# Optimization experiments

Measured on AMD Instinct MI355X. Metric: run time of the kernel, lower is better.

## Reference

```python
import jax, jax.numpy as jnp
import numpy as np

NG, G = 256, 32          # num groups, pedestrians per group
E, H, MID, BN_EPS = 64, 64, 512, 1e-5
BOT = 32

def _bn(x, gamma, beta):
    # training-mode BatchNorm1d applied PER GROUP (axis=1 are the rows of
    # that group's pairwise batch), biased variance, eps=1e-5
    mean = jnp.mean(x, axis=1, keepdims=True)
    var = jnp.mean((x - mean) ** 2, axis=1, keepdims=True)
    return gamma * (x - mean) * jax.lax.rsqrt(var + BN_EPS) + beta

def setup_inputs() -> dict:
    key = jax.random.key(0)
    ks = jax.random.split(key, 8)
    B = NG * G
    starts = np.arange(NG, dtype=np.int64) * G
    seq_start_end = jnp.asarray(np.stack([starts, starts + G], axis=1))
    def lin(k, fi, fo):
        kw, kb = jax.random.split(k)
        lim = 1.0 / np.sqrt(fi)
        return (jax.random.uniform(kw, (fi, fo), jnp.float32, -lim, lim),
                jax.random.uniform(kb, (fo,), jnp.float32, -lim, lim))
    W_spatial, b_spatial = lin(ks[0], 2, E)
    W1, b1 = lin(ks[1], E + H, MID)
    W2, b2 = lin(ks[2], MID, BOT)
    return {
        'h_states': jax.random.normal(ks[3], (1, B, H), jnp.float32),
        'seq_start_end': seq_start_end,
        'end_pos': jax.random.normal(ks[4], (B, 2), jnp.float32),
        'W_spatial': W_spatial, 'b_spatial': b_spatial,
        'W1': W1, 'b1': b1,
        'gamma1': jnp.ones((MID,), jnp.float32), 'beta1': jnp.zeros((MID,), jnp.float32),
        'W2': W2, 'b2': b2,
        'gamma2': jnp.ones((BOT,), jnp.float32), 'beta2': jnp.zeros((BOT,), jnp.float32),
    }

def reference(h_states, seq_start_end, end_pos, W_spatial, b_spatial,
              W1, b1, gamma1, beta1, W2, b2, gamma2, beta2):
    B = end_pos.shape[0]
    ng = seq_start_end.shape[0]
    g = B // ng  # equal-size groups -> fully vectorized
    h = h_states.reshape(B, H).reshape(ng, g, H)
    pos = end_pos.reshape(ng, g, 2)
    # rel[n, i, j] = pos[n, j] - pos[n, i]  (matches repeat/tile in torch code)
    rel = pos[:, None, :, :] - pos[:, :, None, :]            # (ng, g, g, 2)
    emb = rel @ W_spatial + b_spatial                         # (ng, g, g, E)
    hb = jnp.broadcast_to(h[:, None, :, :], (ng, g, g, H))    # hidden of ped j
    x = jnp.concatenate([emb, hb], axis=-1).reshape(ng, g * g, E + H)
    x = jax.nn.relu(_bn(x @ W1 + b1, gamma1, beta1))          # (ng, g*g, 512)
    x = jax.nn.relu(_bn(x @ W2 + b2, gamma2, beta2))          # (ng, g*g, 32)
    pool = x.reshape(ng, g, g, BOT).max(axis=2)               # max over j
    return pool.reshape(B, BOT)
```

## Files before the change

### kernel.cpp

```cpp
#include <hip/hip_runtime.h>

#define GRP 32
#define HD 64
#define MIDD 512
#define LDSTR 520

typedef _Float16 half8 __attribute__((ext_vector_type(8)));
typedef float floatx4 __attribute__((ext_vector_type(4)));

__device__ inline half8 relu8(half8 x) {
    return __builtin_elementwise_max(x, (half8)(_Float16)0);
}

__global__ void prep_wr(const float* __restrict__ Ws, const float* __restrict__ W1,
                        float* __restrict__ wr) {
    int c = blockIdx.x * 64 + threadIdx.x;
    float a0 = 0.f, a1 = 0.f;
#pragma unroll
    for (int e = 0; e < 64; ++e) {
        float w = W1[e * MIDD + c];
        a0 = fmaf(Ws[e], w, a0);
        a1 = fmaf(Ws[64 + e], w, a1);
    }
    wr[c] = a0;
    wr[MIDD + c] = a1;
}

__launch_bounds__(512, 2)
__global__ void pool_main(const float* __restrict__ h_states,
                          const float* __restrict__ end_pos,
                          const float* __restrict__ W1,
                          const float* __restrict__ gamma1,
                          const float* __restrict__ beta1,
                          const float* __restrict__ W2,
                          const float* __restrict__ gamma2,
                          const float* __restrict__ beta2,
                          const float* __restrict__ wr,
                          float* __restrict__ out) {
    __shared__ _Float16 Ash[32][LDSTR];
    __shared__ _Float16 Bsh[32][LDSTR];
    __shared__ _Float16 w2T[32][LDSTR];
    __shared__ float posx[32], posy[32];
    __shared__ float wr0s[512], wr1s[512], g1s[512], be1s[512];
    __shared__ float red[8][2][16][2];
    __shared__ float bns[32], bno[32];

    const int tid  = threadIdx.x;
    const int wave = tid >> 6;
    const int lane = tid & 63;
    const int quad = lane >> 4;
    const int n16  = lane & 15;
    const int g0   = blockIdx.x * GRP;

    wr0s[tid] = wr[tid];
    wr1s[tid] = wr[512 + tid];
    g1s[tid]  = gamma1[tid];
    be1s[tid] = beta1[tid];
    if (tid < 32) {
        posx[tid] = end_pos[(g0 + tid) * 2];
        posy[tid] = end_pos[(g0 + tid) * 2 + 1];
    }
#pragma unroll
    for (int it = 0; it < 32; ++it) {
        int idx = tid + it * 512;
        int k = idx >> 5, nn = idx & 31;
        w2T[nn][k] = (_Float16)W2[idx];
    }
    __syncthreads();

    {
        half8 afr[2][2];
#pragma unroll
        for (int mt = 0; mt < 2; ++mt)
#pragma unroll
            for (int kk = 0; kk < 2; ++kk) {
                const float4* hp = (const float4*)(h_states + (size_t)(g0 + mt * 16 + n16) * HD + kk * 32 + quad * 8);
                float4 p0 = hp[0], p1 = hp[1];
                half8 a;
                a[0] = (_Float16)p0.x; a[1] = (_Float16)p0.y; a[2] = (_Float16)p0.z; a[3] = (_Float16)p0.w;
                a[4] = (_Float16)p1.x; a[5] = (_Float16)p1.y; a[6] = (_Float16)p1.z; a[7] = (_Float16)p1.w;
                afr[mt][kk] = a;
            }

        floatx4 acc[2][4];
#pragma unroll
        for (int a = 0; a < 2; ++a)
#pragma unroll
            for (int b = 0; b < 4; ++b) acc[a][b] = (floatx4){0.f, 0.f, 0.f, 0.f};

#pragma unroll
        for (int nt4 = 0; nt4 < 4; ++nt4) {
            const int c = (wave * 4 + nt4) * 16 + n16;
#pragma unroll
            for (int kk = 0; kk < 2; ++kk) {
                half8 b;
#pragma unroll
                for (int x = 0; x < 8; ++x) {
                    int k = kk * 32 + quad * 8 + x;
                    b[x] = (_Float16)W1[(size_t)(64 + k) * MIDD + c];
                }
#pragma unroll
                for (int mt = 0; mt < 2; ++mt)
                    acc[mt][nt4] = __builtin_amdgcn_mfma_f32_16x16x32_f16(afr[mt][kk], b, acc[mt][nt4], 0, 0, 0);
            }
        }

#pragma unroll
        for (int nt4 = 0; nt4 < 4; ++nt4) {
            const int c = (wave * 4 + nt4) * 16 + n16;
            const float w0 = wr0s[c], w1 = wr1s[c];

            float su = 0.f, ssu = 0.f;
#pragma unroll
            for (int mt = 0; mt < 2; ++mt)
#pragma unroll
                for (int r = 0; r < 4; ++r) {
                    int j = mt * 16 + quad * 4 + r;
                    float u = acc[mt][nt4][r] + posx[j] * w0 + posy[j] * w1;
                    acc[mt][nt4][r] = u;
                    su += u;
                    ssu = fmaf(u, u, ssu);
                }
            su  += __shfl_xor(su, 16);  su  += __shfl_xor(su, 32);
            ssu += __shfl_xor(ssu, 16); ssu += __shfl_xor(ssu, 32);

            float vv[8];
            float sv = 0.f, ssv = 0.f;
#pragma unroll
            for (int ii = 0; ii < 8; ++ii) {
                int i = quad * 8 + ii;
                float v = posx[i] * w0 + posy[i] * w1;
                vv[ii] = v;
                sv += v;
                ssv = fmaf(v, v, ssv);
            }
            sv  += __shfl_xor(sv, 16);  sv  += __shfl_xor(sv, 32);
            ssv += __shfl_xor(ssv, 16); ssv += __shfl_xor(ssv, 32);

            const float muu = su * (1.f / 32.f), muv = sv * (1.f / 32.f);
            const float var = (ssu * (1.f / 32.f) - muu * muu) + (ssv * (1.f / 32.f) - muv * muv);
            const float s    = g1s[c] * rsqrtf(var + 1e-5f);
            const float boff = s * (muu - muv) - be1s[c];

#pragma unroll
            for (int mt = 0; mt < 2; ++mt)
#pragma unroll
                for (int r = 0; r < 4; ++r) {
                    int j = mt * 16 + quad * 4 + r;
                    Ash[j][c] = (_Float16)(s * acc[mt][nt4][r]);
                }
#pragma unroll
            for (int ii = 0; ii < 8; ++ii)
                Bsh[quad * 8 + ii][c] = (_Float16)fmaf(s, vv[ii], boff);
        }
    }
    __syncthreads();

    floatx4 acc2[8][2];
#pragma unroll
    for (int a = 0; a < 8; ++a)
#pragma unroll
        for (int b = 0; b < 2; ++b) acc2[a][b] = (floatx4){0.f, 0.f, 0.f, 0.f};

#pragma unroll 2
    for (int kk = 0; kk < 16; ++kk) {
        const int kb = kk * 32 + quad * 8;
        const half8 w2f0 = *(const half8*)&w2T[n16][kb];
        const half8 w2f1 = *(const half8*)&w2T[16 + n16][kb];
        const half8 a0 = *(const half8*)&Ash[n16][kb];
        const half8 a1 = *(const half8*)&Ash[16 + n16][kb];
#pragma unroll
        for (int mp = 0; mp < 4; ++mp) {
            const int i = wave * 4 + mp;
            const half8 bf = *(const half8*)&Bsh[i][kb];
            const half8 z0 = relu8(a0 - bf);
            const half8 z1 = relu8(a1 - bf);
            acc2[2 * mp][0]     = __builtin_amdgcn_mfma_f32_16x16x32_f16(z0, w2f0, acc2[2 * mp][0], 0, 0, 0);
            acc2[2 * mp][1]     = __builtin_amdgcn_mfma_f32_16x16x32_f16(z0, w2f1, acc2[2 * mp][1], 0, 0, 0);
            acc2[2 * mp + 1][0] = __builtin_amdgcn_mfma_f32_16x16x32_f16(z1, w2f0, acc2[2 * mp + 1][0], 0, 0, 0);
            acc2[2 * mp + 1][1] = __builtin_amdgcn_mfma_f32_16x16x32_f16(z1, w2f1, acc2[2 * mp + 1][1], 0, 0, 0);
        }
    }

    float s0 = 0.f, q0 = 0.f, s1 = 0.f, q1 = 0.f;
#pragma unroll
    for (int mt = 0; mt < 8; ++mt)
#pragma unroll
        for (int r = 0; r < 4; ++r) {
            float v0 = acc2[mt][0][r], v1 = acc2[mt][1][r];
            s0 += v0; q0 = fmaf(v0, v0, q0);
            s1 += v1; q1 = fmaf(v1, v1, q1);
        }
    s0 += __shfl_xor(s0, 16); s0 += __shfl_xor(s0, 32);
    q0 += __shfl_xor(q0, 16); q0 += __shfl_xor(q0, 32);
    s1 += __shfl_xor(s1, 16); s1 += __shfl_xor(s1, 32);
    q1 += __shfl_xor(q1, 16); q1 += __shfl_xor(q1, 32);
    if (lane < 16) {
        red[wave][0][lane][0] = s0; red[wave][0][lane][1] = q0;
        red[wave][1][lane][0] = s1; red[wave][1][lane][1] = q1;
    }
    __syncthreads();
    if (tid < 32) {
        const int nt = tid >> 4, n = tid & 15;
        float s = 0.f, q = 0.f;
#pragma unroll
        for (int w = 0; w < 8; ++w) { s += red[w][nt][n][0]; q += red[w][nt][n][1]; }
        const float mu  = s * (1.f / 1024.f);
        const float var = q * (1.f / 1024.f) - mu * mu;
        const float sc  = gamma2[tid] * rsqrtf(var + 1e-5f);
        bns[tid] = sc;
        bno[tid] = beta2[tid] - sc * mu;
    }
    __syncthreads();

#pragma unroll
    for (int nt = 0; nt < 2; ++nt) {
        const int c = nt * 16 + n16;
        const float sc = bns[c], off = bno[c];
#pragma unroll
        for (int a = 0; a < 4; ++a) {
            float m = 0.f;
#pragma unroll
            for (int p = 0; p < 2; ++p)
#pragma unroll
                for (int r = 0; r < 4; ++r)
                    m = fmaxf(m, fmaf(sc, acc2[2 * a + p][nt][r], off));
            m = fmaxf(m, __shfl_xor(m, 16));
            m = fmaxf(m, __shfl_xor(m, 32));
            if (quad == nt) {
                const int i = wave * 4 + a;
                out[(size_t)(g0 + i) * 32 + c] = m;
            }
        }
    }
}

extern "C" void kernel_launch(void* const* d_in, const int* in_sizes, int n_in,
                              void* d_out, int out_size, void* d_ws, size_t ws_size,
                              hipStream_t stream) {
    (void)in_sizes; (void)n_in; (void)out_size; (void)ws_size;
    const float* h_states  = (const float*)d_in[0];
    const float* end_pos   = (const float*)d_in[2];
    const float* W_spatial = (const float*)d_in[3];
    const float* W1        = (const float*)d_in[5];
    const float* gamma1    = (const float*)d_in[7];
    const float* beta1     = (const float*)d_in[8];
    const float* W2        = (const float*)d_in[9];
    const float* gamma2    = (const float*)d_in[11];
    const float* beta2     = (const float*)d_in[12];
    float* out = (float*)d_out;
    float* wr  = (float*)d_ws;

    prep_wr<<<dim3(8), dim3(64), 0, stream>>>(W_spatial, W1, wr);
    pool_main<<<dim3(256), dim3(512), 0, stream>>>(h_states, end_pos, W1, gamma1, beta1,
                                                   W2, gamma2, beta2, wr, out);
}
```

Before: 99.23 us.

## Split hidden-state GEMM into a separate pre-kernel writing fp16 intermediate

Moves the h·W1 projection out of the main pooling kernel into a new first kernel that writes an fp16 (B×512) intermediate Q to workspace. The wr precompute is folded into that kernel as an extra block. The main kernel now reads Q and computes the BN1 statistics with one thread per column and a serial loop over 32 rows. The goal is to shorten the main kernel and drop the strided per-block W1 loads, at the cost of an extra 8 MB round trip through global memory. It also creates a race: block 256 writes wr inside the same launch, but other blocks do not read wr, so ordering is still correct.

```diff
diff --git a/kernel.cpp b/kernel.cpp
--- a/kernel.cpp
+++ b/kernel.cpp
@@ -12,36 +12,94 @@
     return __builtin_elementwise_max(x, (half8)(_Float16)0);
 }
 
-__global__ void prep_wr(const float* __restrict__ Ws, const float* __restrict__ W1,
-                        float* __restrict__ wr) {
-    int c = blockIdx.x * 64 + threadIdx.x;
-    float a0 = 0.f, a1 = 0.f;
-#pragma unroll
-    for (int e = 0; e < 64; ++e) {
-        float w = W1[e * MIDD + c];
-        a0 = fmaf(Ws[e], w, a0);
-        a1 = fmaf(Ws[64 + e], w, a1);
-    }
-    wr[c] = a0;
-    wr[MIDD + c] = a1;
+__global__ __launch_bounds__(512) void k1(const float* __restrict__ h_states,
+                                          const float* __restrict__ Ws,
+                                          const float* __restrict__ W1,
+                                          _Float16* __restrict__ Q,
+                                          float* __restrict__ wr) {
+    const int tid  = threadIdx.x;
+    if (blockIdx.x == 256) {
+        const int c = tid;
+        float a0 = 0.f, a1 = 0.f;
+#pragma unroll
+        for (int e = 0; e < 64; ++e) {
+            float w = W1[e * MIDD + c];
+            a0 = fmaf(Ws[e], w, a0);
+            a1 = fmaf(Ws[64 + e], w, a1);
+        }
+        wr[c] = a0;
+        wr[MIDD + c] = a1;
+        return;
+    }
+    const int wave = tid >> 6;
+    const int lane = tid & 63;
+    const int quad = lane >> 4;
+    const int n16  = lane & 15;
+    const int r0 = (blockIdx.x >> 3) * 256 + wave * 32;
+    const int c0 = (blockIdx.x & 7) * 64;
+
+    half8 afr[2][2];
+#pragma unroll
+    for (int mt = 0; mt < 2; ++mt)
+#pragma unroll
+        for (int kk = 0; kk < 2; ++kk) {
+            const float4* hp = (const float4*)(h_states + (size_t)(r0 + mt * 16 + n16) * HD + kk * 32 + quad * 8);
+            float4 p0 = hp[0], p1 = hp[1];
+            half8 a;
+            a[0] = (_Float16)p0.x; a[1] = (_Float16)p0.y; a[2] = (_Float16)p0.z; a[3] = (_Float16)p0.w;
+            a[4] = (_Float16)p1.x; a[5] = (_Float16)p1.y; a[6] = (_Float16)p1.z; a[7] = (_Float16)p1.w;
+            afr[mt][kk] = a;
+        }
+
+    floatx4 acc[2][4];
+#pragma unroll
+    for (int a = 0; a < 2; ++a)
+#pragma unroll
+        for (int b = 0; b < 4; ++b) acc[a][b] = (floatx4){0.f, 0.f, 0.f, 0.f};
+
+#pragma unroll
+    for (int nt = 0; nt < 4; ++nt) {
+        const int c = c0 + nt * 16 + n16;
+#pragma unroll
+        for (int kk = 0; kk < 2; ++kk) {
+            half8 b;
+#pragma unroll
+            for (int x = 0; x < 8; ++x) {
+                int k = kk * 32 + quad * 8 + x;
+                b[x] = (_Float16)W1[(size_t)(64 + k) * MIDD + c];
+            }
+#pragma unroll
+            for (int mt = 0; mt < 2; ++mt)
+                acc[mt][nt] = __builtin_amdgcn_mfma_f32_16x16x32_f16(afr[mt][kk], b, acc[mt][nt], 0, 0, 0);
+        }
+    }
+
+#pragma unroll
+    for (int mt = 0; mt < 2; ++mt)
+#pragma unroll
+        for (int nt = 0; nt < 4; ++nt)
+#pragma unroll
+            for (int r = 0; r < 4; ++r) {
+                int row = r0 + mt * 16 + quad * 4 + r;
+                int c   = c0 + nt * 16 + n16;
+                Q[(size_t)row * MIDD + c] = (_Float16)acc[mt][nt][r];
+            }
 }
 
 __launch_bounds__(512, 2)
-__global__ void pool_main(const float* __restrict__ h_states,
-                          const float* __restrict__ end_pos,
-                          const float* __restrict__ W1,
+__global__ void pool_main(const float* __restrict__ end_pos,
+                          const _Float16* __restrict__ Q,
+                          const float* __restrict__ wr,
                           const float* __restrict__ gamma1,
                           const float* __restrict__ beta1,
                           const float* __restrict__ W2,
                           const float* __restrict__ gamma2,
                           const float* __restrict__ beta2,
-                          const float* __restrict__ wr,
                           float* __restrict__ out) {
     __shared__ _Float16 Ash[32][LDSTR];
     __shared__ _Float16 Bsh[32][LDSTR];
     __shared__ _Float16 w2T[32][LDSTR];
     __shared__ float posx[32], posy[32];
-    __shared__ float wr0s[512], wr1s[512], g1s[512], be1s[512];
     __shared__ float red[8][2][16][2];
     __shared__ float bns[32], bno[32];
 
@@ -52,10 +110,6 @@
     const int n16  = lane & 15;
     const int g0   = blockIdx.x * GRP;
 
-    wr0s[tid] = wr[tid];
-    wr1s[tid] = wr[512 + tid];
-    g1s[tid]  = gamma1[tid];
-    be1s[tid] = beta1[tid];
     if (tid < 32) {
         posx[tid] = end_pos[(g0 + tid) * 2];
         posy[tid] = end_pos[(g0 + tid) * 2 + 1];
@@ -69,89 +123,39 @@
     __syncthreads();
 
     {
-        half8 afr[2][2];
-#pragma unroll
-        for (int mt = 0; mt < 2; ++mt)
-#pragma unroll
-            for (int kk = 0; kk < 2; ++kk) {
-                const float4* hp = (const float4*)(h_states + (size_t)(g0 + mt * 16 + n16) * HD + kk * 32 + quad * 8);
-                float4 p0 = hp[0], p1 = hp[1];
-                half8 a;
-                a[0] = (_Float16)p0.x; a[1] = (_Float16)p0.y; a[2] = (_Float16)p0.z; a[3] = (_Float16)p0.w;
-                a[4] = (_Float16)p1.x; a[5] = (_Float16)p1.y; a[6] = (_Float16)p1.z; a[7] = (_Float16)p1.w;
-                afr[mt][kk] = a;
-            }
-
-        floatx4 acc[2][4];
-#pragma unroll
-        for (int a = 0; a < 2; ++a)
-#pragma unroll
-            for (int b = 0; b < 4; ++b) acc[a][b] = (floatx4){0.f, 0.f, 0.f, 0.f};
-
-#pragma unroll
-        for (int nt4 = 0; nt4 < 4; ++nt4) {
-            const int c = (wave * 4 + nt4) * 16 + n16;
-#pragma unroll
-            for (int kk = 0; kk < 2; ++kk) {
-                half8 b;
-#pragma unroll
-                for (int x = 0; x < 8; ++x) {
-                    int k = kk * 32 + quad * 8 + x;
-                    b[x] = (_Float16)W1[(size_t)(64 + k) * MIDD + c];
-                }
-#pragma unroll
-                for (int mt = 0; mt < 2; ++mt)
-                    acc[mt][nt4] = __builtin_amdgcn_mfma_f32_16x16x32_f16(afr[mt][kk], b, acc[mt][nt4], 0, 0, 0);
-            }
-        }
-
-#pragma unroll
-        for (int nt4 = 0; nt4 < 4; ++nt4) {
-            const int c = (wave * 4 + nt4) * 16 + n16;
-            const float w0 = wr0s[c], w1 = wr1s[c];
-
-            float su = 0.f, ssu = 0.f;
-#pragma unroll
-            for (int mt = 0; mt < 2; ++mt)
-#pragma unroll
-                for (int r = 0; r < 4; ++r) {
-                    int j = mt * 16 + quad * 4 + r;
-                    float u = acc[mt][nt4][r] + posx[j] * w0 + posy[j] * w1;
-                    acc[mt][nt4][r] = u;
-                    su += u;
-                    ssu = fmaf(u, u, ssu);
-                }
-            su  += __shfl_xor(su, 16);  su  += __shfl_xor(su, 32);
-            ssu += __shfl_xor(ssu, 16); ssu += __shfl_xor(ssu, 32);
-
-            float vv[8];
-            float sv = 0.f, ssv = 0.f;
-#pragma unroll
-            for (int ii = 0; ii < 8; ++ii) {
-                int i = quad * 8 + ii;
-                float v = posx[i] * w0 + posy[i] * w1;
-                vv[ii] = v;
-                sv += v;
-                ssv = fmaf(v, v, ssv);
-            }
-            sv  += __shfl_xor(sv, 16);  sv  += __shfl_xor(sv, 32);
-            ssv += __shfl_xor(ssv, 16); ssv += __shfl_xor(ssv, 32);
-
-            const float muu = su * (1.f / 32.f), muv = sv * (1.f / 32.f);
-            const float var = (ssu * (1.f / 32.f) - muu * muu) + (ssv * (1.f / 32.f) - muv * muv);
-            const float s    = g1s[c] * rsqrtf(var + 1e-5f);
-            const float boff = s * (muu - muv) - be1s[c];
-
-#pragma unroll
-            for (int mt = 0; mt < 2; ++mt)
-#pragma unroll
-                for (int r = 0; r < 4; ++r) {
-                    int j = mt * 16 + quad * 4 + r;
-                    Ash[j][c] = (_Float16)(s * acc[mt][nt4][r]);
-                }
-#pragma unroll
-            for (int ii = 0; ii < 8; ++ii)
-                Bsh[quad * 8 + ii][c] = (_Float16)fmaf(s, vv[ii], boff);
+        const int c = tid;
+        const float w0 = wr[c], w1 = wr[MIDD + c];
+        const float g  = gamma1[c], be = beta1[c];
+        const _Float16* qp = Q + (size_t)g0 * MIDD + c;
+
+        float uu[32];
+        float su = 0.f, ssu = 0.f;
+#pragma unroll
+        for (int j = 0; j < 32; ++j) {
+            float u = (float)qp[(size_t)j * MIDD] + posx[j] * w0 + posy[j] * w1;
+            uu[j] = u;
+            su += u;
+            ssu = fmaf(u, u, ssu);
+        }
+        float sv = 0.f, ssv = 0.f;
+#pragma unroll
+        for (int i = 0; i < 32; ++i) {
+            float v = posx[i] * w0 + posy[i] * w1;
+            sv += v;
+            ssv = fmaf(v, v, ssv);
+        }
+        const float muu = su * (1.f / 32.f), muv = sv * (1.f / 32.f);
+        const float var = (ssu * (1.f / 32.f) - muu * muu) + (ssv * (1.f / 32.f) - muv * muv);
+        const float s    = g * rsqrtf(var + 1e-5f);
+        const float boff = s * (muu - muv) - be;
+
+#pragma unroll
+        for (int j = 0; j < 32; ++j)
+            Ash[j][c] = (_Float16)(s * uu[j]);
+#pragma unroll
+        for (int i = 0; i < 32; ++i) {
+            float v = posx[i] * w0 + posy[i] * w1;
+            Bsh[i][c] = (_Float16)fmaf(s, v, boff);
         }
     }
     __syncthreads();
@@ -249,9 +253,11 @@
     const float* gamma2    = (const float*)d_in[11];
     const float* beta2     = (const float*)d_in[12];
     float* out = (float*)d_out;
-    float* wr  = (float*)d_ws;
-
-    prep_wr<<<dim3(8), dim3(64), 0, stream>>>(W_spatial, W1, wr);
-    pool_main<<<dim3(256), dim3(512), 0, stream>>>(h_states, end_pos, W1, gamma1, beta1,
-                                                   W2, gamma2, beta2, wr, out);
-}
+
+    float*    wr = (float*)d_ws;
+    _Float16* Q  = (_Float16*)((char*)d_ws + 4096);
+
+    k1<<<dim3(257), dim3(512), 0, stream>>>(h_states, W_spatial, W1, Q, wr);
+    pool_main<<<dim3(256), dim3(512), 0, stream>>>(end_pos, Q, wr, gamma1, beta1,
+                                                   W2, gamma2, beta2, out);
+}
```

Measured after the change: 103.9 us. +4.7%, slower.
